# Kernel tuning notes

Measured on AMD Instinct MI355X. Metric: run time of the kernel, lower is better.

## Reference

```python
import jax, jax.numpy as jnp
import numpy as np

RES = 7          # pooler resolution
RATIO = 2        # sampling ratio
LEVEL_STRIDES = (4, 8, 16, 32)
NUM_CLASSES = 4
BINS = 8
EPS = 1e-5


def roi_align_one(feat, boxes, scale):
    """feat: [C,H,W]; boxes: [N,4] (t,l,b,r) in image coords. Returns [N,C,RES,RES]."""
    C, H, W = feat.shape
    P = RES * RATIO
    t = boxes[:, 0] * scale - 0.5
    l = boxes[:, 1] * scale - 0.5
    b = boxes[:, 2] * scale - 0.5
    r = boxes[:, 3] * scale - 0.5
    bin_h = (b - t) / RES
    bin_w = (r - l) / RES
    grid = (jnp.arange(P, dtype=feat.dtype) + 0.5) / RATIO      # [P] bin-unit offsets
    ys = jnp.clip(t[:, None] + bin_h[:, None] * grid, 0.0, H - 1.0)  # [N,P]
    xs = jnp.clip(l[:, None] + bin_w[:, None] * grid, 0.0, W - 1.0)  # [N,P]
    y0 = jnp.floor(ys).astype(jnp.int32)
    x0 = jnp.floor(xs).astype(jnp.int32)
    y1 = jnp.minimum(y0 + 1, H - 1)
    x1 = jnp.minimum(x0 + 1, W - 1)
    wy = (ys - y0.astype(feat.dtype))[:, :, None]   # [N,P,1]
    wx = (xs - x0.astype(feat.dtype))[:, None, :]   # [N,1,P]

    def g(yi, xi):  # -> [C,N,P,P]
        return feat[:, yi[:, :, None], xi[:, None, :]]

    v = (g(y0, x0) * (1 - wy) * (1 - wx) + g(y0, x1) * (1 - wy) * wx
         + g(y1, x0) * wy * (1 - wx) + g(y1, x1) * wy * wx)      # [C,N,P,P]
    v = v.reshape(C, -1, RES, RATIO, RES, RATIO).mean(axis=(3, 5))  # avg-pool bins
    return jnp.transpose(v, (1, 0, 2, 3))


def setup_inputs():
    key = jax.random.key(0)
    ks = jax.random.split(key, 16)
    B, N, C, FC = 2, 256, 256, 1024
    f0 = jax.random.normal(ks[0], (B, C, 128, 128), jnp.float32)
    f1 = jax.random.normal(ks[1], (B, C, 64, 64), jnp.float32)
    f2 = jax.random.normal(ks[2], (B, C, 32, 32), jnp.float32)
    f3 = jax.random.normal(ks[3], (B, C, 16, 16), jnp.float32)
    yx = jax.random.uniform(ks[4], (B, N, 2), jnp.float32) * 384.0 + 64.0
    hw = jax.random.uniform(ks[5], (B, N, 2), jnp.float32) * 96.0 + 32.0
    bbox2d = jnp.concatenate([yx, hw], axis=-1)            # yxhw
    anchor_id = jax.random.randint(ks[6], (B, N, 1), 0, 12, jnp.int32)
    zeropad = (jax.random.uniform(ks[7], (B, N, 1)) > 0.1).astype(jnp.float32)
    in_dim = C * RES * RES
    fc1_w = jax.random.normal(ks[8], (FC, in_dim), jnp.float32) / np.sqrt(in_dim)
    fc2_w = jax.random.normal(ks[9], (FC, FC), jnp.float32) / np.sqrt(FC)
    out_ch = NUM_CLASSES * (1 + 6 + 2 * BINS) + 1           # 93
    pred_w = jax.random.normal(ks[10], (out_ch, FC), jnp.float32) * 0.01
    return dict(f0=f0, f1=f1, f2=f2, f3=f3, bbox2d=bbox2d, anchor_id=anchor_id,
                zeropad=zeropad,
                fc1_w=fc1_w, fc1_b=jnp.zeros((FC,)), bn1_g=jnp.ones((FC,)), bn1_b=jnp.zeros((FC,)),
                fc2_w=fc2_w, fc2_b=jnp.zeros((FC,)), bn2_g=jnp.ones((FC,)), bn2_b=jnp.zeros((FC,)),
                pred_w=pred_w, pred_b=jnp.zeros((out_ch,)))


def reference(f0, f1, f2, f3, bbox2d, anchor_id, zeropad,
              fc1_w, fc1_b, bn1_g, bn1_b, fc2_w, fc2_b, bn2_g, bn2_b, pred_w, pred_b):
    feats = [f0, f1, f2, f3]
    B, N, _ = bbox2d.shape
    y, x, h, w = [bbox2d[..., i] for i in range(4)]
    tlbr = jnp.stack([y - h / 2, x - w / 2, y + h / 2, x + w / 2], axis=-1)  # [B,N,4]
    level = anchor_id[..., 0] // 3                                          # [B,N]

    # Route each proposal to its FPN level: compute roi-align per level, select by mask.
    pooled = 0.0
    for i, stride in enumerate(LEVEL_STRIDES):
        roi = jax.vmap(lambda f, bx, s=stride: roi_align_one(f, bx, 1.0 / s))(feats[i], tlbr)  # [B,N,C,R,R]
        mask = (level == i).astype(roi.dtype)[..., None, None, None]
        pooled = pooled + roi * mask

    xflat = pooled.reshape(B * N, -1)
    for w_, b_, g_, be_ in [(fc1_w, fc1_b, bn1_g, bn1_b), (fc2_w, fc2_b, bn2_g, bn2_b)]:
        xflat = xflat @ w_.T + b_
        mu = xflat.mean(axis=0)
        var = xflat.var(axis=0)
        xflat = (xflat - mu) * jax.lax.rsqrt(var + EPS) * g_ + be_   # BatchNorm1d (train mode)
        xflat = jax.nn.relu(xflat)
    pred = (xflat @ pred_w.T + pred_b).reshape(B, N, -1) * zeropad    # [B,N,93]
    strides = level.astype(pred.dtype)[..., None] * zeropad           # [B,N,1]

    # decode: slice per-loss channels (category: NC+1; others: NC*dims)
    ctgr_logit = pred[..., 0:NUM_CLASSES + 1]                                  # [B,N,5]
    d3 = pred[..., 5:5 + NUM_CLASSES * 6].reshape(B, N, NUM_CLASSES, 6)
    o = 5 + NUM_CLASSES * 6
    yaw_cls = pred[..., o:o + NUM_CLASSES * BINS].reshape(B, N, NUM_CLASSES, BINS)
    o += NUM_CLASSES * BINS
    yaw_res = pred[..., o:o + NUM_CLASSES * BINS].reshape(B, N, NUM_CLASSES, BINS)

    # apply 3d box deltas per class (vectorized over class dim)
    anc = bbox2d[:, :, None, :]                     # [B,N,1,4] yxhw
    st = 4.0 * jnp.exp2(strides)                    # [B,N,1] anchor stride in px
    cy = anc[..., 0] + d3[..., 0] * anc[..., 2]
    cx = anc[..., 1] + d3[..., 1] * anc[..., 3]
    nh = anc[..., 2] * jnp.exp(d3[..., 2])
    nw = anc[..., 3] * jnp.exp(d3[..., 3])
    z = d3[..., 4] * st
    ln = jnp.exp(d3[..., 5]) * st
    bbox3d = jnp.stack([cy, cx, z, nh, nw, ln], axis=-1)  # [B,N,NC,6]

    out = jnp.concatenate([
        bbox3d.reshape(B, N, -1),                         # 24
        jax.nn.softmax(ctgr_logit, axis=-1),              # 5
        jax.nn.softmax(yaw_cls, axis=-1).reshape(B, N, -1),  # 32
        (jax.nn.sigmoid(yaw_res) * 0.6 - 0.3).reshape(B, N, -1),  # 32
    ], axis=-1)                                           # [B,N,93]
    return out
```

## Files before the change

kernel.cpp:

```cpp
#include <hip/hip_runtime.h>
#include <cstdint>
#include <cstddef>

typedef __attribute__((ext_vector_type(8))) short bf16x8;
typedef __attribute__((ext_vector_type(4))) float f32x4;
typedef __attribute__((ext_vector_type(4))) int   i32x4;

#define C_CH   256
#define NBOX   512
#define FCDIM  1024
#define K1     12544
#define OUTC   93
#define Z1     14
#define Z2     8

__device__ __forceinline__ unsigned short f2bf(float f) {
    unsigned u = __float_as_uint(f);
    u += 0x7fffu + ((u >> 16) & 1u);
    return (unsigned short)(u >> 16);
}
__device__ __forceinline__ float bf2f(short s) {
    return __uint_as_float((unsigned)(unsigned short)s << 16);
}
__device__ __forceinline__ void stage16(const short* g, const short* l) {
    __builtin_amdgcn_global_load_lds(
        (const __attribute__((address_space(1))) void*)g,
        (__attribute__((address_space(3))) void*)l, 16, 0, 0);
}

__global__ __launch_bounds__(256) void cast_bf16_kernel(
    const float* __restrict__ in, short* __restrict__ out, int n8)
{
    int i = blockIdx.x * 256 + threadIdx.x;
    if (i >= n8) return;
    const float4* p = (const float4*)(in + (size_t)i * 8);
    float4 a = p[0], b = p[1];
    union { unsigned short s[8]; i32x4 v; } u;
    u.s[0] = f2bf(a.x); u.s[1] = f2bf(a.y); u.s[2] = f2bf(a.z); u.s[3] = f2bf(a.w);
    u.s[4] = f2bf(b.x); u.s[5] = f2bf(b.y); u.s[6] = f2bf(b.z); u.s[7] = f2bf(b.w);
    *(i32x4*)(out + (size_t)i * 8) = u.v;
}

__global__ __launch_bounds__(256) void transpose_all_kernel(
    const float* __restrict__ f0, const float* __restrict__ f1,
    const float* __restrict__ f2, const float* __restrict__ f3,
    short* __restrict__ g0, short* __restrict__ g1,
    short* __restrict__ g2, short* __restrict__ g3)
{
    __shared__ short tile[128 * 66];
    int id = blockIdx.x;
    const float* src; short* dst; int HW, nx;
    if (id < 1024)      { src = f0; dst = g0; HW = 16384; nx = 128; }
    else if (id < 1280) { id -= 1024; src = f1; dst = g1; HW = 4096; nx = 32; }
    else if (id < 1344) { id -= 1280; src = f2; dst = g2; HW = 1024; nx = 8; }
    else                { id -= 1344; src = f3; dst = g3; HW = 256;  nx = 2; }
    int xb = id % nx;  int rest = id / nx;
    int cy = rest & 3; int b = rest >> 2;
    int p0 = xb * 128, c0 = cy * 64;

    const float* s = src + ((size_t)b * C_CH + c0) * HW + p0;
    int t = threadIdx.x;
    #pragma unroll
    for (int it = 0; it < 16; ++it) {
        int slot = it * 256 + t;
        int cl = slot >> 6;
        int pp = slot & 63;
        float2 v = *(const float2*)(s + (size_t)cl * HW + pp * 2);
        tile[(pp * 2) * 66 + cl]     = (short)f2bf(v.x);
        tile[(pp * 2 + 1) * 66 + cl] = (short)f2bf(v.y);
    }
    __syncthreads();
    short* d = dst + ((size_t)b * HW + p0) * C_CH + c0;
    #pragma unroll
    for (int it = 0; it < 16; ++it) {
        int pl = it * 8 + (t >> 5);
        int c2 = (t & 31) * 2;
        *(unsigned*)(d + (size_t)pl * C_CH + c2) = *(const unsigned*)&tile[pl * 66 + c2];
    }
}

__global__ __launch_bounds__(512) void roi_kernel(
    const short* __restrict__ g0, const short* __restrict__ g1,
    const short* __restrict__ g2, const short* __restrict__ g3,
    const float* __restrict__ bbox, const int* __restrict__ aid,
    short* __restrict__ pooled)
{
    int bn  = blockIdx.x;
    int b   = bn >> 8;
    int t   = threadIdx.x;
    int c   = t & 255;
    int sub = t >> 8;

    __shared__ int   xo0[14], xo1[14];
    __shared__ float wxs[14];
    __shared__ int   yo0[14], yo1[14];
    __shared__ float wys[14];
    __shared__ short otile[K1];

    float yb = bbox[bn*4+0], xb = bbox[bn*4+1], hb = bbox[bn*4+2], wb = bbox[bn*4+3];
    int level = aid[bn] / 3;
    const short* gsrc = (level == 0) ? g0 : (level == 1) ? g1 : (level == 2) ? g2 : g3;
    int H = 128 >> level;
    float scale = 1.0f / (float)(4 << level);
    const short* gp = gsrc + (size_t)b * H * H * C_CH;

    if (t < 14) {
        float g  = ((float)t + 0.5f) * 0.5f;
        float l0 = (xb - 0.5f*wb) * scale - 0.5f;
        float bw = wb * scale * (1.0f/7.0f);
        float v  = fminf(fmaxf(l0 + bw * g, 0.0f), (float)(H-1));
        int i0 = (int)v;
        xo0[t] = i0 * C_CH;
        xo1[t] = min(i0 + 1, H - 1) * C_CH;
        wxs[t] = v - (float)i0;
    } else if (t < 28) {
        int sy = t - 14;
        float g  = ((float)sy + 0.5f) * 0.5f;
        float t0 = (yb - 0.5f*hb) * scale - 0.5f;
        float bh = hb * scale * (1.0f/7.0f);
        float v  = fminf(fmaxf(t0 + bh * g, 0.0f), (float)(H-1));
        int i0 = (int)v;
        yo0[sy] = i0 * H * C_CH;
        yo1[sy] = min(i0 + 1, H - 1) * H * C_CH;
        wys[sy] = v - (float)i0;
    }
    __syncthreads();

    #pragma unroll 2
    for (int s = sub; s < 49; s += 2) {
        int py = s / 7, px = s - py * 7;
        float acc = 0.0f;
        #pragma unroll
        for (int i = 0; i < 2; i++) {
            int sy = 2 * py + i;
            int ry0 = yo0[sy], ry1 = yo1[sy];
            float wy = wys[sy];
            #pragma unroll
            for (int j = 0; j < 2; j++) {
                int sx = 2 * px + j;
                int cx0 = xo0[sx] + c, cx1 = xo1[sx] + c;
                float wx = wxs[sx];
                float v00 = bf2f(gp[ry0 + cx0]);
                float v01 = bf2f(gp[ry0 + cx1]);
                float v10 = bf2f(gp[ry1 + cx0]);
                float v11 = bf2f(gp[ry1 + cx1]);
                float top = v00 * (1.0f - wx) + v01 * wx;
                float bot = v10 * (1.0f - wx) + v11 * wx;
                acc += top * (1.0f - wy) + bot * wy;
            }
        }
        otile[c * 49 + s] = (short)f2bf(acc * 0.25f);
    }
    __syncthreads();

    const i32x4* srcv = (const i32x4*)otile;
    i32x4* dstv = (i32x4*)(pooled + (size_t)bn * K1);
    for (int j = t; j < (K1 * 2) / 16; j += 512)
        dstv[j] = srcv[j];
}

__global__ __launch_bounds__(256) void gemm_db(
    const short* __restrict__ A, const short* __restrict__ Bt,
    float* __restrict__ part, int K, int KC, int NP)
{
    __shared__ short As[2][4096];
    __shared__ short Bs[2][4096];
    int t = threadIdx.x, lane = t & 63, w = t >> 6;
    int bid = blockIdx.x;
    int p = bid % NP, m = bid / NP;
    int n = p & 7, z = p >> 3;
    int m0 = m * 128, n0 = n * 128;
    size_t k0 = (size_t)z * KC;

    int gslot = (lane & 3) * 8;
    int lrow  = lane >> 2;
    int qa0 = 2 * w, qa1 = 2 * w + 1;
    const short* gA0 = A  + (size_t)(m0 + qa0 * 16 + lrow) * K + k0 + gslot;
    const short* gA1 = A  + (size_t)(m0 + qa1 * 16 + lrow) * K + k0 + gslot;
    const short* gB0 = Bt + (size_t)(n0 + qa0 * 16 + lrow) * K + k0 + gslot;
    const short* gB1 = Bt + (size_t)(n0 + qa1 * 16 + lrow) * K + k0 + gslot;
    const short* lA0 = &As[0][qa0 * 512];
    const short* lA1 = &As[0][qa1 * 512];
    const short* lB0 = &Bs[0][qa0 * 512];
    const short* lB1 = &Bs[0][qa1 * 512];

    int wr = (w >> 1) * 64, wc = (w & 1) * 64;
    int fr = lane & 15, kg = lane >> 4;
    int raoff = (wr + fr) * 32 + kg * 8;
    int rboff = (wc + fr) * 32 + kg * 8;

    int nsteps = KC >> 5;

    stage16(gA0, lA0); stage16(gA1, lA1);
    stage16(gB0, lB0); stage16(gB1, lB1);
    __syncthreads();

    f32x4 acc[4][4] = {};
    for (int s = 0; s < nsteps; ++s) {
        int cur = s & 1;
        if (s + 1 < nsteps) {
            int nxt = cur ^ 1;
            int ks = (s + 1) * 32;
            stage16(gA0 + ks, lA0 + nxt * 4096);
            stage16(gA1 + ks, lA1 + nxt * 4096);
            stage16(gB0 + ks, lB0 + nxt * 4096);
            stage16(gB1 + ks, lB1 + nxt * 4096);
        }
        const short* ra = &As[cur][raoff];
        const short* rb = &Bs[cur][rboff];
        bf16x8 af[4], bm[4];
        #pragma unroll
        for (int i = 0; i < 4; i++) af[i] = *(const bf16x8*)(ra + i * 512);
        #pragma unroll
        for (int j = 0; j < 4; j++) bm[j] = *(const bf16x8*)(rb + j * 512);
        #pragma unroll
        for (int i = 0; i < 4; i++)
            #pragma unroll
            for (int j = 0; j < 4; j++)
                acc[i][j] = __builtin_amdgcn_mfma_f32_16x16x32_bf16(af[i], bm[j], acc[i][j], 0, 0, 0);
        __syncthreads();
    }

    float* base = part + (size_t)z * NBOX * FCDIM;
    #pragma unroll
    for (int i = 0; i < 4; i++)
        #pragma unroll
        for (int j = 0; j < 4; j++)
            #pragma unroll
            for (int r = 0; r < 4; r++) {
                int row = m0 + wr + i * 16 + kg * 4 + r;
                int col = n0 + wc + j * 16 + fr;
                base[(size_t)row * FCDIM + col] = acc[i][j][r];
            }
}

template<int NZ>
__global__ __launch_bounds__(256) void bn_stats1(
    const float* __restrict__ part, float* __restrict__ xsum, float* __restrict__ pstat)
{
    int tc = threadIdx.x & 63;
    int tr = threadIdx.x >> 6;
    int c  = blockIdx.x * 64 + tc;
    int r0 = blockIdx.y * 32;
    const size_t P = (size_t)NBOX * FCDIM;

    float s = 0.0f, q = 0.0f;
    #pragma unroll
    for (int rr = 0; rr < 8; rr++) {
        size_t o = (size_t)(r0 + tr + rr * 4) * FCDIM + c;
        float x = 0.0f;
        #pragma unroll
        for (int z = 0; z < NZ; z++) x += part[o + (size_t)z * P];
        xsum[o] = x;
        s += x; q += x * x;
    }
    __shared__ float Ss[4][64], Sq[4][64];
    Ss[tr][tc] = s; Sq[tr][tc] = q;
    __syncthreads();
    if (tr == 0) {
        float S = Ss[0][tc] + Ss[1][tc] + Ss[2][tc] + Ss[3][tc];
        float Q = Sq[0][tc] + Sq[1][tc] + Sq[2][tc] + Sq[3][tc];
        pstat[blockIdx.y * FCDIM + c] = S;
        pstat[16 * FCDIM + blockIdx.y * FCDIM + c] = Q;
    }
}

__global__ __launch_bounds__(256) void bn_stats2(
    const float* __restrict__ pstat, const float* __restrict__ g,
    const float* __restrict__ be, float* __restrict__ scsh)
{
    int c = blockIdx.x * 256 + threadIdx.x;
    float S = 0.0f, Q = 0.0f;
    #pragma unroll
    for (int i = 0; i < 16; i++) {
        S += pstat[i * FCDIM + c];
        Q += pstat[16 * FCDIM + i * FCDIM + c];
    }
    float mu  = S * (1.0f / NBOX);
    float var = Q * (1.0f / NBOX) - mu * mu;
    float a = g[c] * rsqrtf(var + 1e-5f);
    scsh[c]         = a;
    scsh[FCDIM + c] = be[c] - mu * a;
}

template<bool BF>
__global__ __launch_bounds__(256) void bn_apply(
    const float* __restrict__ xsum, const float* __restrict__ scsh,
    short* __restrict__ obf, float* __restrict__ of)
{
    size_t base = ((size_t)blockIdx.x * 256 + threadIdx.x) * 8;
    int c0 = (int)(base & (FCDIM - 1));
    float4 x0 = *(const float4*)(xsum + base);
    float4 x1 = *(const float4*)(xsum + base + 4);
    float4 a0 = *(const float4*)(scsh + c0);
    float4 a1 = *(const float4*)(scsh + c0 + 4);
    float4 b0 = *(const float4*)(scsh + FCDIM + c0);
    float4 b1 = *(const float4*)(scsh + FCDIM + c0 + 4);
    float r[8];
    r[0] = fmaxf(x0.x*a0.x + b0.x, 0.0f);
    r[1] = fmaxf(x0.y*a0.y + b0.y, 0.0f);
    r[2] = fmaxf(x0.z*a0.z + b0.z, 0.0f);
    r[3] = fmaxf(x0.w*a0.w + b0.w, 0.0f);
    r[4] = fmaxf(x1.x*a1.x + b1.x, 0.0f);
    r[5] = fmaxf(x1.y*a1.y + b1.y, 0.0f);
    r[6] = fmaxf(x1.z*a1.z + b1.z, 0.0f);
    r[7] = fmaxf(x1.w*a1.w + b1.w, 0.0f);
    if (BF) {
        union { unsigned short s[8]; i32x4 v; } u;
        #pragma unroll
        for (int i = 0; i < 8; i++) u.s[i] = f2bf(r[i]);
        *(i32x4*)(obf + base) = u.v;
    } else {
        *(float4*)(of + base)     = *(float4*)&r[0];
        *(float4*)(of + base + 4) = *(float4*)&r[4];
    }
}

__global__ __launch_bounds__(128) void pred_kernel(
    const float* __restrict__ xin, const float* __restrict__ pw,
    const float* __restrict__ pb, const float* __restrict__ bbox,
    const int* __restrict__ aid, const float* __restrict__ zp,
    float* __restrict__ out)
{
    int bn = blockIdx.x;
    int t  = threadIdx.x;
    __shared__ float xs[FCDIM];
    __shared__ float pr[OUTC];
    for (int i = t; i < FCDIM; i += 128)
        xs[i] = xin[(size_t)bn * FCDIM + i];
    __syncthreads();

    float z = zp[bn];
    if (t < OUTC) {
        const float* wrow = pw + (size_t)t * FCDIM;
        float acc = 0.0f;
        for (int k = 0; k < FCDIM; k += 4) {
            float4 w4 = *(const float4*)(wrow + k);
            acc += xs[k] * w4.x + xs[k+1] * w4.y + xs[k+2] * w4.z + xs[k+3] * w4.w;
        }
        pr[t] = (acc + pb[t]) * z;
    }
    __syncthreads();

    if (t < OUTC) {
        float y = bbox[bn*4+0], x = bbox[bn*4+1], h = bbox[bn*4+2], w = bbox[bn*4+3];
        int lvl = aid[bn] / 3;
        float st = 4.0f * exp2f((float)lvl * z);
        float o;
        if (t < 24) {
            int k = t / 6, j = t - k * 6;
            const float* d = &pr[5 + k * 6];
            switch (j) {
                case 0:  o = y + d[0] * h;  break;
                case 1:  o = x + d[1] * w;  break;
                case 2:  o = d[4] * st;     break;
                case 3:  o = h * expf(d[2]); break;
                case 4:  o = w * expf(d[3]); break;
                default: o = expf(d[5]) * st; break;
            }
        } else if (t < 29) {
            float m = pr[0];
            #pragma unroll
            for (int i = 1; i < 5; i++) m = fmaxf(m, pr[i]);
            float den = 0.0f;
            #pragma unroll
            for (int i = 0; i < 5; i++) den += expf(pr[i] - m);
            o = expf(pr[t - 24] - m) / den;
        } else if (t < 61) {
            int i = t - 29, k = i >> 3;
            const float* qq = &pr[29 + k * 8];
            float m = qq[0];
            #pragma unroll
            for (int ii = 1; ii < 8; ii++) m = fmaxf(m, qq[ii]);
            float den = 0.0f;
            #pragma unroll
            for (int ii = 0; ii < 8; ii++) den += expf(qq[ii] - m);
            o = expf(pr[t] - m) / den;
        } else {
            o = 1.0f / (1.0f + expf(-pr[t])) * 0.6f - 0.3f;
        }
        out[(size_t)bn * OUTC + t] = o;
    }
}

extern "C" void kernel_launch(void* const* d_in, const int* in_sizes, int n_in,
                              void* d_out, int out_size, void* d_ws, size_t ws_size,
                              hipStream_t stream)
{
    const float* f0   = (const float*)d_in[0];
    const float* f1   = (const float*)d_in[1];
    const float* f2   = (const float*)d_in[2];
    const float* f3   = (const float*)d_in[3];
    const float* bbox = (const float*)d_in[4];
    const int*   aid  = (const int*)d_in[5];
    const float* zp   = (const float*)d_in[6];
    const float* fc1w = (const float*)d_in[7];
    const float* bn1g = (const float*)d_in[9];
    const float* bn1b = (const float*)d_in[10];
    const float* fc2w = (const float*)d_in[11];
    const float* bn2g = (const float*)d_in[13];
    const float* bn2b = (const float*)d_in[14];
    const float* pw   = (const float*)d_in[15];
    const float* pb   = (const float*)d_in[16];
    float* out = (float*)d_out;

    char* ws = (char*)d_ws;
    short* pooled = (short*)(ws);
    short* gt0    = (short*)(ws + 13631488);
    short* gt1    = (short*)(ws + 30408704);
    short* gt2    = (short*)(ws + 34603008);
    short* gt3    = (short*)(ws + 35651584);
    short* w1     = (short*)(ws + 36700160);
    short* w2     = (short*)(ws + 62390272);
    float* part1  = (float*)(ws + 64487424);
    float* part2  = (float*)(ws + 123207680);
    float* xsum   = (float*)(ws + 139984896);
    short* x1n    = (short*)(ws + 142082048);
    float* x2n    = (float*)(ws + 143130624);
    float* pstat  = (float*)(ws + 145227776);
    float* scsh   = (float*)(ws + 145358848);

    transpose_all_kernel<<<1360, 256, 0, stream>>>(f0, f1, f2, f3, gt0, gt1, gt2, gt3);

    roi_kernel<<<NBOX, 512, 0, stream>>>(gt0, gt1, gt2, gt3, bbox, aid, pooled);

    cast_bf16_kernel<<<(K1 * FCDIM / 8 + 255) / 256, 256, 0, stream>>>(fc1w, w1, K1 * FCDIM / 8);

    gemm_db<<<4 * 8 * Z1, 256, 0, stream>>>(pooled, w1, part1, K1, K1 / Z1, 8 * Z1);

    cast_bf16_kernel<<<(FCDIM * FCDIM / 8 + 255) / 256, 256, 0, stream>>>(fc2w, w2, FCDIM * FCDIM / 8);

    bn_stats1<Z1><<<dim3(16, 16), 256, 0, stream>>>(part1, xsum, pstat);
    bn_stats2<<<4, 256, 0, stream>>>(pstat, bn1g, bn1b, scsh);
    bn_apply<true><<<256, 256, 0, stream>>>(xsum, scsh, x1n, nullptr);

    gemm_db<<<4 * 8 * Z2, 256, 0, stream>>>(x1n, w2, part2, FCDIM, FCDIM / Z2, 8 * Z2);

    bn_stats1<Z2><<<dim3(16, 16), 256, 0, stream>>>(part2, xsum, pstat);
    bn_stats2<<<4, 256, 0, stream>>>(pstat, bn2g, bn2b, scsh);
    bn_apply<false><<<256, 256, 0, stream>>>(xsum, scsh, nullptr, x2n);

    pred_kernel<<<NBOX, 128, 0, stream>>>(x2n, pw, pb, bbox, aid, zp, out);
}
```

Before: 138.4 us.

## Fuse weight bf16 cast into GEMM and merge BN stat/apply kernels

The separate fp32-to-bf16 weight cast kernels are removed. The GEMM now stages fp32 weight tiles into LDS with an XOR swizzle and converts them to bf16 in registers before each MFMA. The two-kernel BN statistics are merged through a last-block atomic counter, and the second BN apply is folded into the prediction kernel. This drops several launches and a full write/read pass over the 50MB fc1 weight, but doubles LDS traffic for B and adds per-step conversion ALU work inside the GEMM loop.

After: 183.4 us. 1.33x slower.

```diff
diff --git a/kernel.cpp b/kernel.cpp
--- a/kernel.cpp
+++ b/kernel.cpp
@@ -22,33 +22,22 @@
 __device__ __forceinline__ float bf2f(short s) {
     return __uint_as_float((unsigned)(unsigned short)s << 16);
 }
-__device__ __forceinline__ void stage16(const short* g, const short* l) {
+__device__ __forceinline__ void stage16(const void* g, const void* l) {
     __builtin_amdgcn_global_load_lds(
         (const __attribute__((address_space(1))) void*)g,
         (__attribute__((address_space(3))) void*)l, 16, 0, 0);
-}
-
-__global__ __launch_bounds__(256) void cast_bf16_kernel(
-    const float* __restrict__ in, short* __restrict__ out, int n8)
-{
-    int i = blockIdx.x * 256 + threadIdx.x;
-    if (i >= n8) return;
-    const float4* p = (const float4*)(in + (size_t)i * 8);
-    float4 a = p[0], b = p[1];
-    union { unsigned short s[8]; i32x4 v; } u;
-    u.s[0] = f2bf(a.x); u.s[1] = f2bf(a.y); u.s[2] = f2bf(a.z); u.s[3] = f2bf(a.w);
-    u.s[4] = f2bf(b.x); u.s[5] = f2bf(b.y); u.s[6] = f2bf(b.z); u.s[7] = f2bf(b.w);
-    *(i32x4*)(out + (size_t)i * 8) = u.v;
 }
 
 __global__ __launch_bounds__(256) void transpose_all_kernel(
     const float* __restrict__ f0, const float* __restrict__ f1,
     const float* __restrict__ f2, const float* __restrict__ f3,
     short* __restrict__ g0, short* __restrict__ g1,
-    short* __restrict__ g2, short* __restrict__ g3)
+    short* __restrict__ g2, short* __restrict__ g3,
+    unsigned* __restrict__ counters)
 {
     __shared__ short tile[128 * 66];
     int id = blockIdx.x;
+    if (id == 0 && threadIdx.x < 2) counters[threadIdx.x] = 0;
     const float* src; short* dst; int HW, nx;
     if (id < 1024)      { src = f0; dst = g0; HW = 16384; nx = 128; }
     else if (id < 1280) { id -= 1024; src = f1; dst = g1; HW = 4096; nx = 32; }
@@ -159,12 +148,12 @@
         dstv[j] = srcv[j];
 }
 
-__global__ __launch_bounds__(256) void gemm_db(
-    const short* __restrict__ A, const short* __restrict__ Bt,
+__global__ __launch_bounds__(256) void gemm_f32b(
+    const short* __restrict__ A, const float* __restrict__ Bw,
     float* __restrict__ part, int K, int KC, int NP)
 {
     __shared__ short As[2][4096];
-    __shared__ short Bs[2][4096];
+    __shared__ float Bsf[2][4096];
     int t = threadIdx.x, lane = t & 63, w = t >> 6;
     int bid = blockIdx.x;
     int p = bid % NP, m = bid / NP;
@@ -172,27 +161,35 @@
     int m0 = m * 128, n0 = n * 128;
     size_t k0 = (size_t)z * KC;
 
-    int gslot = (lane & 3) * 8;
-    int lrow  = lane >> 2;
     int qa0 = 2 * w, qa1 = 2 * w + 1;
-    const short* gA0 = A  + (size_t)(m0 + qa0 * 16 + lrow) * K + k0 + gslot;
-    const short* gA1 = A  + (size_t)(m0 + qa1 * 16 + lrow) * K + k0 + gslot;
-    const short* gB0 = Bt + (size_t)(n0 + qa0 * 16 + lrow) * K + k0 + gslot;
-    const short* gB1 = Bt + (size_t)(n0 + qa1 * 16 + lrow) * K + k0 + gslot;
+    const short* gA0 = A + (size_t)(m0 + qa0 * 16 + (lane >> 2)) * K + k0 + (lane & 3) * 8;
+    const short* gA1 = A + (size_t)(m0 + qa1 * 16 + (lane >> 2)) * K + k0 + (lane & 3) * 8;
     const short* lA0 = &As[0][qa0 * 512];
     const short* lA1 = &As[0][qa1 * 512];
-    const short* lB0 = &Bs[0][qa0 * 512];
-    const short* lB1 = &Bs[0][qa1 * 512];
+
+    const float* gB[4];
+    const float* lB[4];
+    int swslot = ((lane & 7) ^ (lane >> 3)) * 4;
+    #pragma unroll
+    for (int j = 0; j < 4; j++) {
+        int q = 4 * w + j;
+        gB[j] = Bw + (size_t)(n0 + q * 8 + (lane >> 3)) * K + k0 + swslot;
+        lB[j] = &Bsf[0][q * 256];
+    }
 
     int wr = (w >> 1) * 64, wc = (w & 1) * 64;
     int fr = lane & 15, kg = lane >> 4;
     int raoff = (wr + fr) * 32 + kg * 8;
-    int rboff = (wc + fr) * 32 + kg * 8;
+    int s0 = (kg * 2) ^ (fr & 7);
+    int s1 = s0 ^ 1;
+    int rb0 = (wc + fr) * 32 + s0 * 4;
+    int rb1 = (wc + fr) * 32 + s1 * 4;
 
     int nsteps = KC >> 5;
 
     stage16(gA0, lA0); stage16(gA1, lA1);
-    stage16(gB0, lB0); stage16(gB1, lB1);
+    #pragma unroll
+    for (int j = 0; j < 4; j++) stage16(gB[j], lB[j]);
     __syncthreads();
 
     f32x4 acc[4][4] = {};
@@ -203,16 +200,21 @@
             int ks = (s + 1) * 32;
             stage16(gA0 + ks, lA0 + nxt * 4096);
             stage16(gA1 + ks, lA1 + nxt * 4096);
-            stage16(gB0 + ks, lB0 + nxt * 4096);
-            stage16(gB1 + ks, lB1 + nxt * 4096);
-        }
-        const short* ra = &As[cur][raoff];
-        const short* rb = &Bs[cur][rboff];
+            #pragma unroll
+            for (int j = 0; j < 4; j++) stage16(gB[j] + ks, lB[j] + nxt * 4096);
+        }
         bf16x8 af[4], bm[4];
         #pragma unroll
-        for (int i = 0; i < 4; i++) af[i] = *(const bf16x8*)(ra + i * 512);
-        #pragma unroll
-        for (int j = 0; j < 4; j++) bm[j] = *(const bf16x8*)(rb + j * 512);
+        for (int i = 0; i < 4; i++) af[i] = *(const bf16x8*)(&As[cur][raoff + i * 512]);
+        #pragma unroll
+        for (int j = 0; j < 4; j++) {
+            f32x4 lo = *(const f32x4*)(&Bsf[cur][rb0 + j * 512]);
+            f32x4 hi = *(const f32x4*)(&Bsf[cur][rb1 + j * 512]);
+            union { unsigned short us[8]; bf16x8 v; } ub;
+            #pragma unroll
+            for (int e = 0; e < 4; e++) { ub.us[e] = f2bf(lo[e]); ub.us[4 + e] = f2bf(hi[e]); }
+            bm[j] = ub.v;
+        }
         #pragma unroll
         for (int i = 0; i < 4; i++)
             #pragma unroll
@@ -235,8 +237,10 @@
 }
 
 template<int NZ>
-__global__ __launch_bounds__(256) void bn_stats1(
-    const float* __restrict__ part, float* __restrict__ xsum, float* __restrict__ pstat)
+__global__ __launch_bounds__(256) void bn_stats(
+    const float* __restrict__ part, float* __restrict__ xsum, float* __restrict__ pstat,
+    const float* __restrict__ g, const float* __restrict__ be,
+    float* __restrict__ scsh, unsigned* __restrict__ counter)
 {
     int tc = threadIdx.x & 63;
     int tr = threadIdx.x >> 6;
@@ -263,30 +267,32 @@
         pstat[blockIdx.y * FCDIM + c] = S;
         pstat[16 * FCDIM + blockIdx.y * FCDIM + c] = Q;
     }
-}
-
-__global__ __launch_bounds__(256) void bn_stats2(
-    const float* __restrict__ pstat, const float* __restrict__ g,
-    const float* __restrict__ be, float* __restrict__ scsh)
-{
-    int c = blockIdx.x * 256 + threadIdx.x;
-    float S = 0.0f, Q = 0.0f;
-    #pragma unroll
-    for (int i = 0; i < 16; i++) {
-        S += pstat[i * FCDIM + c];
-        Q += pstat[16 * FCDIM + i * FCDIM + c];
-    }
-    float mu  = S * (1.0f / NBOX);
-    float var = Q * (1.0f / NBOX) - mu * mu;
-    float a = g[c] * rsqrtf(var + 1e-5f);
-    scsh[c]         = a;
-    scsh[FCDIM + c] = be[c] - mu * a;
-}
-
-template<bool BF>
-__global__ __launch_bounds__(256) void bn_apply(
+    __shared__ unsigned last;
+    __threadfence();
+    __syncthreads();
+    if (threadIdx.x == 0) last = (atomicAdd(counter, 1u) == 255u) ? 1u : 0u;
+    __syncthreads();
+    if (last) {
+        __threadfence();
+        for (int ci = threadIdx.x; ci < FCDIM; ci += 256) {
+            float S = 0.0f, Q = 0.0f;
+            #pragma unroll
+            for (int i = 0; i < 16; i++) {
+                S += pstat[i * FCDIM + ci];
+                Q += pstat[16 * FCDIM + i * FCDIM + ci];
+            }
+            float mu  = S * (1.0f / NBOX);
+            float var = Q * (1.0f / NBOX) - mu * mu;
+            float a = g[ci] * rsqrtf(var + 1e-5f);
+            scsh[ci]         = a;
+            scsh[FCDIM + ci] = be[ci] - mu * a;
+        }
+    }
+}
+
+__global__ __launch_bounds__(256) void bn_apply_bf(
     const float* __restrict__ xsum, const float* __restrict__ scsh,
-    short* __restrict__ obf, float* __restrict__ of)
+    short* __restrict__ obf)
 {
     size_t base = ((size_t)blockIdx.x * 256 + threadIdx.x) * 8;
     int c0 = (int)(base & (FCDIM - 1));
@@ -305,29 +311,24 @@
     r[5] = fmaxf(x1.y*a1.y + b1.y, 0.0f);
     r[6] = fmaxf(x1.z*a1.z + b1.z, 0.0f);
     r[7] = fmaxf(x1.w*a1.w + b1.w, 0.0f);
-    if (BF) {
-        union { unsigned short s[8]; i32x4 v; } u;
-        #pragma unroll
-        for (int i = 0; i < 8; i++) u.s[i] = f2bf(r[i]);
-        *(i32x4*)(obf + base) = u.v;
-    } else {
-        *(float4*)(of + base)     = *(float4*)&r[0];
-        *(float4*)(of + base + 4) = *(float4*)&r[4];
-    }
-}
-
-__global__ __launch_bounds__(128) void pred_kernel(
-    const float* __restrict__ xin, const float* __restrict__ pw,
-    const float* __restrict__ pb, const float* __restrict__ bbox,
-    const int* __restrict__ aid, const float* __restrict__ zp,
-    float* __restrict__ out)
+    union { unsigned short s[8]; i32x4 v; } u;
+    #pragma unroll
+    for (int i = 0; i < 8; i++) u.s[i] = f2bf(r[i]);
+    *(i32x4*)(obf + base) = u.v;
+}
+
+__global__ __launch_bounds__(128) void bn2_pred_kernel(
+    const float* __restrict__ xsum, const float* __restrict__ scsh,
+    const float* __restrict__ pw, const float* __restrict__ pb,
+    const float* __restrict__ bbox, const int* __restrict__ aid,
+    const float* __restrict__ zp, float* __restrict__ out)
 {
     int bn = blockIdx.x;
     int t  = threadIdx.x;
     __shared__ float xs[FCDIM];
     __shared__ float pr[OUTC];
     for (int i = t; i < FCDIM; i += 128)
-        xs[i] = xin[(size_t)bn * FCDIM + i];
+        xs[i] = fmaxf(xsum[(size_t)bn * FCDIM + i] * scsh[i] + scsh[FCDIM + i], 0.0f);
     __syncthreads();
 
     float z = zp[bn];
@@ -410,35 +411,26 @@
     short* gt1    = (short*)(ws + 30408704);
     short* gt2    = (short*)(ws + 34603008);
     short* gt3    = (short*)(ws + 35651584);
-    short* w1     = (short*)(ws + 36700160);
-    short* w2     = (short*)(ws + 62390272);
-    float* part1  = (float*)(ws + 64487424);
-    float* part2  = (float*)(ws + 123207680);
-    float* xsum   = (float*)(ws + 139984896);
-    short* x1n    = (short*)(ws + 142082048);
-    float* x2n    = (float*)(ws + 143130624);
-    float* pstat  = (float*)(ws + 145227776);
-    float* scsh   = (float*)(ws + 145358848);
-
-    transpose_all_kernel<<<1360, 256, 0, stream>>>(f0, f1, f2, f3, gt0, gt1, gt2, gt3);
+    float* part1  = (float*)(ws + 36700160);
+    float* part2  = (float*)(ws + 66060288);
+    float* xsum   = (float*)(ws + 82837504);
+    short* x1n    = (short*)(ws + 84934656);
+    float* pstat  = (float*)(ws + 85983232);
+    float* scsh   = (float*)(ws + 86114304);
+    unsigned* cnt = (unsigned*)(ws + 86122496);
+
+    transpose_all_kernel<<<1360, 256, 0, stream>>>(f0, f1, f2, f3, gt0, gt1, gt2, gt3, cnt);
 
     roi_kernel<<<NBOX, 512, 0, stream>>>(gt0, gt1, gt2, gt3, bbox, aid, pooled);
 
-    cast_bf16_kernel<<<(K1 * FCDIM / 8 + 255) / 256, 256, 0, stream>>>(fc1w, w1, K1 * FCDIM / 8);
-
-    gemm_db<<<4 * 8 * Z1, 256, 0, stream>>>(pooled, w1, part1, K1, K1 / Z1, 8 * Z1);
-
-    cast_bf16_kernel<<<(FCDIM * FCDIM / 8 + 255) / 256, 256, 0, stream>>>(fc2w, w2, FCDIM * FCDIM / 8);
-
-    bn_stats1<Z1><<<dim3(16, 16), 256, 0, stream>>>(part1, xsum, pstat);
-    bn_stats2<<<4, 256, 0, stream>>>(pstat, bn1g, bn1b, scsh);
-    bn_apply<true><<<256, 256, 0, stream>>>(xsum, scsh, x1n, nullptr);
-
-    gemm_db<<<4 * 8 * Z2, 256, 0, stream>>>(x1n, w2, part2, FCDIM, FCDIM / Z2, 8 * Z2);
-
-    bn_stats1<Z2><<<dim3(16, 16), 256, 0, stream>>>(part2, xsum, pstat);
-    bn_stats2<<<4, 256, 0, stream>>>(pstat, bn2g, bn2b, scsh);
-    bn_apply<false><<<256, 256, 0, stream>>>(xsum, scsh, nullptr, x2n);
-
-    pred_kernel<<<NBOX, 128, 0, stream>>>(x2n, pw, pb, bbox, aid, zp, out);
-}
+    gemm_f32b<<<4 * 8 * Z1, 256, 0, stream>>>(pooled, fc1w, part1, K1, K1 / Z1, 8 * Z1);
+
+    bn_stats<Z1><<<dim3(16, 16), 256, 0, stream>>>(part1, xsum, pstat, bn1g, bn1b, scsh, cnt);
+    bn_apply_bf<<<256, 256, 0, stream>>>(xsum, scsh, x1n);
+
+    gemm_f32b<<<4 * 8 * Z2, 256, 0, stream>>>(x1n, fc2w, part2, FCDIM, FCDIM / Z2, 8 * Z2);
+
+    bn_stats<Z2><<<dim3(16, 16), 256, 0, stream>>>(part2, xsum, pstat, bn2g, bn2b, scsh, cnt + 1);
+
+    bn2_pred_kernel<<<NBOX, 128, 0, stream>>>(xsum, scsh, pw, pb, bbox, aid, zp, out);
+}
```
